# Performance work log

Hardware: AMD Instinct MI355X
Metric: run time of the kernel (lower is better)

The kernel has to match this reference:

```python
import jax, jax.numpy as jnp
import numpy as np

B, S, D_MODEL, H = 4, 2048, 1024, 16
DEPTH = D_MODEL // H          # 64
HD = DEPTH // 2               # 32, per-head projection dim
SCALE = float(np.sqrt(DEPTH))  # note: sqrt(full depth), as in the torch code
NEG = -1e10


def setup_inputs() -> dict:
    key = jax.random.key(0)
    kq, kk, kv, km, kwq, kwk, kwv, kwo = jax.random.split(key, 8)
    q = jax.random.normal(kq, (B, S, D_MODEL), dtype=jnp.float32)
    k = jax.random.normal(kk, (B, S, D_MODEL), dtype=jnp.float32)
    v = jax.random.normal(kv, (B, S, D_MODEL), dtype=jnp.float32)
    attention_mask = jax.random.uniform(km, (B, S, S)) < 0.1
    # xavier-uniform-ish init; stacked per-head weights [H, d_model, hd]
    lim_qkv = float(np.sqrt(6.0 / (D_MODEL + HD)))
    Wq = jax.random.uniform(kwq, (H, D_MODEL, HD), minval=-lim_qkv, maxval=lim_qkv)
    Wk = jax.random.uniform(kwk, (H, D_MODEL, HD), minval=-lim_qkv, maxval=lim_qkv)
    Wv = jax.random.uniform(kwv, (H, D_MODEL, HD), minval=-lim_qkv, maxval=lim_qkv)
    lim_o = float(np.sqrt(6.0 / (H * HD + D_MODEL)))
    Wo = jax.random.uniform(kwo, (H * HD, D_MODEL), minval=-lim_o, maxval=lim_o)
    return {"q": q, "k": k, "v": v, "attention_mask": attention_mask,
            "Wq": Wq, "Wk": Wk, "Wv": Wv, "Wo": Wo}


def reference(q, k, v, attention_mask, Wq, Wk, Wv, Wo):
    # batched per-head projections (equivalent to the per-head Linear loop)
    Q = jnp.einsum('bsd,hde->bhse', q, Wq)   # [B,H,S,hd]
    K = jnp.einsum('bsd,hde->bhse', k, Wk)
    V = jnp.einsum('bsd,hde->bhse', v, Wv)
    scores = jnp.einsum('bhqe,bhke->bhqk', Q, K) / SCALE  # [B,H,S,S]
    scores = jnp.where(attention_mask[:, None, :, :], NEG, scores)
    attn = jax.nn.softmax(scores, axis=-1)
    z = jnp.einsum('bhqk,bhke->bhqe', attn, V)            # [B,H,S,hd]
    # concat heads along last dim (head order matches torch cat)
    multi = z.transpose(0, 2, 1, 3).reshape(q.shape[0], q.shape[1], H * HD)
    out = multi @ Wo                                       # [B,S,d_model]
    return out  # dropout p=0.0 (eval) is identity
```

## Files before the change

### kernel.cpp

```cpp
#include <hip/hip_runtime.h>
#include <hip/hip_bf16.h>
#include <math.h>

typedef unsigned short u16;
typedef unsigned int u32;
typedef unsigned long long u64;
typedef __attribute__((ext_vector_type(8))) short s16x8;
typedef __attribute__((ext_vector_type(4))) short s16x4;
typedef __attribute__((ext_vector_type(4))) float f32x4;
typedef __attribute__((ext_vector_type(16))) float f32x16;
typedef __attribute__((ext_vector_type(2))) unsigned int u32x2;

#define DEV static __device__ __forceinline__

DEV u16 f2bf(float f){
  __hip_bfloat16 h = __float2bfloat16(f);
  return *reinterpret_cast<u16*>(&h);
}

DEV u32 cvt_pk_bf16(float lo, float hi_){
  u32 r;
  asm("v_cvt_pk_bf16_f32 %0, %1, %2" : "=v"(r) : "v"(lo), "v"(hi_));
  return r;
}

DEV u32x2 pl32swap(u32 a, u32 b){
  return __builtin_amdgcn_permlane32_swap(a, b, false, false);
}

template<int CPOS> DEV float mzero(float p, u32 msn){
  int ext;
  asm("v_bfe_i32 %0, %1, %2, 1" : "=v"(ext) : "v"(msn), "n"(CPOS));
  return __uint_as_float(__float_as_uint(p) & (u32)ext);
}

__global__ void detect_mask_kernel(const unsigned char* __restrict__ m, int* __restrict__ flag){
  __shared__ int cnt;
  if (threadIdx.x==0) cnt=0;
  __syncthreads();
  int nz=0;
  for (int i=threadIdx.x;i<4096;i+=256) nz += (m[(size_t)i*4+1]!=0)?1:0;
  if (nz) atomicAdd(&cnt, nz);
  __syncthreads();
  if (threadIdx.x==0) *flag = (cnt==0)?4:1;
}

__global__ __launch_bounds__(256) void pack_mask_kernel(const unsigned char* __restrict__ m,
    const int* __restrict__ flag, u16* __restrict__ mb16){
  const int stride = *flag;
  const size_t gid = (size_t)blockIdx.x*256u + threadIdx.x;
  u32 bits = 0;
  if (stride == 1){
    const uint4 v = *(const uint4*)(m + gid*16);
    bits  =  ((v.x & 0x01010101u) * 0x01020408u) >> 24;
    bits |= (((v.y & 0x01010101u) * 0x01020408u) >> 24) << 4;
    bits |= (((v.z & 0x01010101u) * 0x01020408u) >> 24) << 8;
    bits |= (((v.w & 0x01010101u) * 0x01020408u) >> 24) << 12;
  } else {
    const unsigned char* mm = m + gid*64;
    const uint4 a = *(const uint4*)(mm);
    const uint4 b = *(const uint4*)(mm+16);
    const uint4 c = *(const uint4*)(mm+32);
    const uint4 d = *(const uint4*)(mm+48);
    bits  = (u32)(a.x!=0) | ((u32)(a.y!=0)<<1) | ((u32)(a.z!=0)<<2) | ((u32)(a.w!=0)<<3)
          | ((u32)(b.x!=0)<<4) | ((u32)(b.y!=0)<<5) | ((u32)(b.z!=0)<<6) | ((u32)(b.w!=0)<<7)
          | ((u32)(c.x!=0)<<8) | ((u32)(c.y!=0)<<9) | ((u32)(c.z!=0)<<10)| ((u32)(c.w!=0)<<11)
          | ((u32)(d.x!=0)<<12)| ((u32)(d.y!=0)<<13)| ((u32)(d.z!=0)<<14)| ((u32)(d.w!=0)<<15);
  }
  mb16[gid] = (u16)bits;
}

__global__ __launch_bounds__(256) void prep_weights_kernel(
    const float* __restrict__ Wq, const float* __restrict__ Wk, const float* __restrict__ Wv,
    const float* __restrict__ Wo, u16* __restrict__ WT, u16* __restrict__ WoT){
  int gid = blockIdx.x*256 + threadIdx.x;
  if (gid < 3*512*1024){
    int z = gid >> 19;
    int r = gid & ((1<<19)-1);
    int n = r >> 10, d = r & 1023;
    const float* W = (z==0)?Wq:((z==1)?Wk:Wv);
    int h = n>>5, e = n&31;
    float wv = W[((size_t)h*1024 + (size_t)d)*32 + e];
    if (z==0) wv *= 0.18033688011112042f;
    WT[gid] = f2bf(wv);
  } else {
    int r = gid - 3*512*1024;
    int n = r >> 9, cc = r & 511;
    WoT[r] = f2bf(Wo[(size_t)cc*1024 + n]);
  }
}

__global__ __launch_bounds__(256) void gemm_proj_kernel(
    const float* __restrict__ Aq, const float* __restrict__ Ak, const float* __restrict__ Av,
    const u16* __restrict__ WT, u16* __restrict__ Qp, u16* __restrict__ Kp, u16* __restrict__ Vt)
{
  __shared__ u16 As[128*64];
  __shared__ u16 Bs[128*64];
  const int z = blockIdx.z;
  const float* __restrict__ A = (z==0)?Aq:((z==1)?Ak:Av);
  const u16* __restrict__ W = WT + (size_t)z*(512*1024);
  const int m0 = blockIdx.x*128, n0 = blockIdx.y*128;
  const int t = threadIdx.x, lane = t&63, wv = t>>6;
  const int wr = wv>>1, wc = wv&1;
  const int c = lane&15, g = lane>>4;
  f32x4 acc[4][4] = {};
  for (int kk=0; kk<1024; kk+=64){
    #pragma unroll
    for (int j=0;j<8;j++){
      int idx = t + j*256;
      int row = idx>>4, kq=(idx&15)<<2;
      f32x4 a4 = *(const f32x4*)(A + (size_t)(m0+row)*1024 + kk + kq);
      s16x4 b4;
      b4[0]=(short)f2bf(a4[0]); b4[1]=(short)f2bf(a4[1]);
      b4[2]=(short)f2bf(a4[2]); b4[3]=(short)f2bf(a4[3]);
      int co = (kq<<1) ^ ((row&7)<<4);
      *(s16x4*)((char*)As + row*128 + co) = b4;
    }
    #pragma unroll
    for (int j=0;j<4;j++){
      int idx = t + j*256;
      int n = idx>>3, k8=(idx&7)<<3;
      s16x8 bv = *(const s16x8*)(W + (size_t)(n0+n)*1024 + kk + k8);
      int co = (k8<<1) ^ ((n&7)<<4);
      *(s16x8*)((char*)Bs + n*128 + co) = bv;
    }
    __syncthreads();
    #pragma unroll
    for (int ks=0;ks<2;ks++){
      s16x8 af[4], bf[4];
      #pragma unroll
      for (int i=0;i<4;i++){
        int ra = wr*64 + i*16 + c;
        af[i] = *(const s16x8*)((const char*)As + ra*128 + ((ks*64 + g*16) ^ ((ra&7)<<4)));
        int rb = wc*64 + i*16 + c;
        bf[i] = *(const s16x8*)((const char*)Bs + rb*128 + ((ks*64 + g*16) ^ ((rb&7)<<4)));
      }
      #pragma unroll
      for (int mi=0;mi<4;mi++)
        #pragma unroll
        for (int nj=0;nj<4;nj++)
          acc[mi][nj] = __builtin_amdgcn_mfma_f32_16x16x32_bf16(af[mi], bf[nj], acc[mi][nj], 0, 0, 0);
    }
    __syncthreads();
  }
  #pragma unroll
  for (int mi=0;mi<4;mi++){
    #pragma unroll
    for (int nj=0;nj<4;nj++){
      #pragma unroll
      for (int r=0;r<4;r++){
        int gm = m0 + wr*64 + mi*16 + g*4 + r;
        int gn = n0 + wc*64 + nj*16 + c;
        u16 val = f2bf(acc[mi][nj][r]);
        int b = gm>>11, s = gm&2047, hh = gn>>5, e = gn&31;
        if (z==0)      Qp[((size_t)(b*16+hh)*2048 + s)*32 + e] = val;
        else if (z==1) Kp[((size_t)(b*16+hh)*2048 + s)*32 + e] = val;
        else           Vt[((size_t)(b*16+hh)*32 + e)*2048 + s] = val;
      }
    }
  }
}

__global__ __launch_bounds__(256, 4) void attn_kernel(
    const u16* __restrict__ Qp, const u16* __restrict__ Kp, const u16* __restrict__ Vt,
    const u32* __restrict__ mb32, u16* __restrict__ Z)
{
  __shared__ float Osh[4][32][36];
  const int t = threadIdx.x, lane = t&63, wid = t>>6;
  const int c = lane&31, hi = lane>>5;
  const int hi8 = hi*8;
  const int wg = blockIdx.x;
  const int xcd = wg & 7, loc = wg >> 3;
  const int bh = xcd*8 + (loc>>4);
  const int qb = loc & 15;
  const int b = bh>>4, h = bh&15;
  const int q0 = qb*128 + wid*32;
  const u16* Qh = Qp + (size_t)bh*2048*32;
  const u16* Kh = Kp + (size_t)bh*2048*32;
  const u16* Vh = Vt + (size_t)bh*32*2048;

  const s16x8 qf0 = *(const s16x8*)(Qh + (size_t)(q0 + c)*32 + hi8);
  const s16x8 qf1 = *(const s16x8*)(Qh + (size_t)(q0 + c)*32 + 16 + hi8);

  union { u32 u[4]; s16x8 v; } ones_u = {{0x3F803F80u,0x3F803F80u,0x3F803F80u,0x3F803F80u}};
  const s16x8 ones = ones_u.v;

  const f32x16 z16 = {0,0,0,0,0,0,0,0,0,0,0,0,0,0,0,0};
  f32x16 O = z16, L = z16;
  const u32* mrowp = mb32 + ((size_t)b*2048 + (size_t)(q0 + c))*64;

  #pragma unroll 2
  for (int kt = 0; kt < 64; ++kt){
    const int kb = kt*32;
    const u16* kbase = Kh + (size_t)(kb + c)*32 + hi8;
    const s16x8 kf0 = *(const s16x8*)(kbase);
    const s16x8 kf1 = *(const s16x8*)(kbase + 16);
    const u16* vbase = Vh + (size_t)c*2048 + kb + hi8;
    const s16x8 vf0 = *(const s16x8*)(vbase);
    const s16x8 vf1 = *(const s16x8*)(vbase + 16);
    const u32 msn = ~(mrowp[kt] >> (4*hi));

    f32x16 p = __builtin_amdgcn_mfma_f32_32x32x16_bf16(kf0, qf0, z16, 0, 0, 0);
    p = __builtin_amdgcn_mfma_f32_32x32x16_bf16(kf1, qf1, p, 0, 0, 0);

    #define MZE(R) p[R] = mzero<(((R)&3)+8*((R)>>2))>(__builtin_amdgcn_exp2f(p[R]), msn)
    MZE(0);  MZE(1);  MZE(2);  MZE(3);
    MZE(4);  MZE(5);  MZE(6);  MZE(7);
    MZE(8);  MZE(9);  MZE(10); MZE(11);
    MZE(12); MZE(13); MZE(14); MZE(15);
    #undef MZE

    u32 pw0 = cvt_pk_bf16(p[0],  p[1]);
    u32 pw1 = cvt_pk_bf16(p[2],  p[3]);
    u32 pw2 = cvt_pk_bf16(p[4],  p[5]);
    u32 pw3 = cvt_pk_bf16(p[6],  p[7]);
    u32 pw4 = cvt_pk_bf16(p[8],  p[9]);
    u32 pw5 = cvt_pk_bf16(p[10], p[11]);
    u32 pw6 = cvt_pk_bf16(p[12], p[13]);
    u32 pw7 = cvt_pk_bf16(p[14], p[15]);
    u32x2 a02 = pl32swap(pw0, pw2);
    u32x2 a13 = pl32swap(pw1, pw3);
    u32x2 a46 = pl32swap(pw4, pw6);
    u32x2 a57 = pl32swap(pw5, pw7);
    union { u32 u[4]; s16x8 v; } fA0 = {{a02[0], a13[0], a02[1], a13[1]}};
    union { u32 u[4]; s16x8 v; } fA1 = {{a46[0], a57[0], a46[1], a57[1]}};

    O = __builtin_amdgcn_mfma_f32_32x32x16_bf16(vf0, fA0.v, O, 0, 0, 0);
    O = __builtin_amdgcn_mfma_f32_32x32x16_bf16(vf1, fA1.v, O, 0, 0, 0);
    L = __builtin_amdgcn_mfma_f32_32x32x16_bf16(ones, fA0.v, L, 0, 0, 0);
    L = __builtin_amdgcn_mfma_f32_32x32x16_bf16(ones, fA1.v, L, 0, 0, 0);
  }

  const float linv = 1.0f / L[0];
  #pragma unroll
  for (int r=0;r<16;r++){
    const int hd = (r&3) + 8*(r>>2) + 4*hi;
    Osh[wid][c][hd] = O[r] * linv;
  }
  __syncthreads();
  const int rq = lane >> 1, rc0 = (lane & 1)*16;
  const float* orow = &Osh[wid][rq][0];
  union { u16 q[8]; s16x8 v; } o0, o1;
  #pragma unroll
  for (int j=0;j<8;j++){ o0.q[j] = f2bf(orow[rc0+j]); o1.q[j] = f2bf(orow[rc0+8+j]); }
  u16* zp = Z + ((size_t)b*2048 + (size_t)(q0 + rq))*512 + h*32 + rc0;
  *(s16x8*)(zp)   = o0.v;
  *(s16x8*)(zp+8) = o1.v;
}

__global__ __launch_bounds__(256) void gemm_out_kernel(
    const u16* __restrict__ Zb, const u16* __restrict__ WoT, float* __restrict__ out)
{
  __shared__ u16 As[128*64];
  __shared__ u16 Bs[128*64];
  const int m0 = blockIdx.x*128, n0 = blockIdx.y*128;
  const int t = threadIdx.x, lane=t&63, wv=t>>6;
  const int wr=wv>>1, wc=wv&1, c=lane&15, g=lane>>4;
  f32x4 acc[4][4] = {};
  for (int kk=0; kk<512; kk+=64){
    #pragma unroll
    for (int j=0;j<4;j++){
      int idx = t + j*256;
      int row = idx>>3, k8=(idx&7)<<3;
      int co = (k8<<1) ^ ((row&7)<<4);
      s16x8 av = *(const s16x8*)(Zb + (size_t)(m0+row)*512 + kk + k8);
      *(s16x8*)((char*)As + row*128 + co) = av;
      s16x8 bv = *(const s16x8*)(WoT + (size_t)(n0+row)*512 + kk + k8);
      *(s16x8*)((char*)Bs + row*128 + co) = bv;
    }
    __syncthreads();
    #pragma unroll
    for (int ks=0;ks<2;ks++){
      s16x8 af[4], bf[4];
      #pragma unroll
      for (int i=0;i<4;i++){
        int ra = wr*64 + i*16 + c;
        af[i] = *(const s16x8*)((const char*)As + ra*128 + ((ks*64 + g*16) ^ ((ra&7)<<4)));
        int rb = wc*64 + i*16 + c;
        bf[i] = *(const s16x8*)((const char*)Bs + rb*128 + ((ks*64 + g*16) ^ ((rb&7)<<4)));
      }
      #pragma unroll
      for (int mi=0;mi<4;mi++)
        #pragma unroll
        for (int nj=0;nj<4;nj++)
          acc[mi][nj] = __builtin_amdgcn_mfma_f32_16x16x32_bf16(af[mi], bf[nj], acc[mi][nj], 0, 0, 0);
    }
    __syncthreads();
  }
  #pragma unroll
  for (int mi=0;mi<4;mi++)
    #pragma unroll
    for (int nj=0;nj<4;nj++)
      #pragma unroll
      for (int r=0;r<4;r++){
        int gm = m0 + wr*64 + mi*16 + g*4 + r;
        int gn = n0 + wc*64 + nj*16 + c;
        out[(size_t)gm*1024 + gn] = acc[mi][nj][r];
      }
}

extern "C" void kernel_launch(void* const* d_in, const int* in_sizes, int n_in,
                              void* d_out, int out_size, void* d_ws, size_t ws_size,
                              hipStream_t stream)
{
  const float* q  = (const float*)d_in[0];
  const float* k  = (const float*)d_in[1];
  const float* v  = (const float*)d_in[2];
  const unsigned char* mask = (const unsigned char*)d_in[3];
  const float* Wq = (const float*)d_in[4];
  const float* Wk = (const float*)d_in[5];
  const float* Wv = (const float*)d_in[6];
  const float* Wo = (const float*)d_in[7];
  float* out = (float*)d_out;

  char* ws = (char*)d_ws;
  u16* Qp  = (u16*)(ws);
  u16* Kp  = (u16*)(ws + 8388608);
  u16* Vt  = (u16*)(ws + 16777216);
  u16* Z   = (u16*)(ws + 25165824);
  u16* WT  = (u16*)(ws + 33554432);
  u16* WoT = (u16*)(ws + 36700160);
  u16* mb16 = (u16*)(ws + 37748736);
  int* flag = (int*)(ws + 39845888);

  detect_mask_kernel<<<1, 256, 0, stream>>>(mask, flag);
  pack_mask_kernel<<<4096, 256, 0, stream>>>(mask, flag, mb16);
  prep_weights_kernel<<<8192, 256, 0, stream>>>(Wq, Wk, Wv, Wo, WT, WoT);
  gemm_proj_kernel<<<dim3(64,4,3), 256, 0, stream>>>(q, k, v, WT, Qp, Kp, Vt);
  attn_kernel<<<1024, 256, 0, stream>>>(Qp, Kp, Vt, (const u32*)mb16, Z);
  gemm_out_kernel<<<dim3(64,8), 256, 0, stream>>>(Z, WoT, out);
  (void)in_sizes; (void)n_in; (void)out_size; (void)ws_size;
}
```

Before: 220.8 us.

## Split attention key range across two waves per query tile and combine in LDS

Each 32-row query tile is now handled by two waves, each covering half of the key tiles. Their partial O and L accumulators are summed through shared memory before normalisation. The grid doubles to 2048 blocks and the launch bound asks for 8 blocks per CU, which shortens each wave's serial loop and exposes more parallelism. The cost is extra LDS traffic, an additional barrier, and half the waves sitting idle during the epilogue. This relies on the kernel not subtracting a running max, so the two halves can be added without rescaling.

```diff
diff --git a/kernel.cpp b/kernel.cpp
--- a/kernel.cpp
+++ b/kernel.cpp
@@ -161,20 +161,23 @@
   }
 }
 
-__global__ __launch_bounds__(256, 4) void attn_kernel(
+__global__ __launch_bounds__(256, 8) void attn_kernel(
     const u16* __restrict__ Qp, const u16* __restrict__ Kp, const u16* __restrict__ Vt,
     const u32* __restrict__ mb32, u16* __restrict__ Z)
 {
-  __shared__ float Osh[4][32][36];
+  __shared__ float Psh[2][32][33];
+  __shared__ float Tsh[2][32][33];
+  __shared__ float Lsh[2][32];
   const int t = threadIdx.x, lane = t&63, wid = t>>6;
   const int c = lane&31, hi = lane>>5;
   const int hi8 = hi*8;
+  const int qt = wid>>1, kh = wid&1;
   const int wg = blockIdx.x;
   const int xcd = wg & 7, loc = wg >> 3;
-  const int bh = xcd*8 + (loc>>4);
-  const int qb = loc & 15;
+  const int bh = xcd*8 + (loc>>5);
+  const int qg = loc & 31;
   const int b = bh>>4, h = bh&15;
-  const int q0 = qb*128 + wid*32;
+  const int q0 = qg*64 + qt*32;
   const u16* Qh = Qp + (size_t)bh*2048*32;
   const u16* Kh = Kp + (size_t)bh*2048*32;
   const u16* Vh = Vt + (size_t)bh*32*2048;
@@ -188,9 +191,10 @@
   const f32x16 z16 = {0,0,0,0,0,0,0,0,0,0,0,0,0,0,0,0};
   f32x16 O = z16, L = z16;
   const u32* mrowp = mb32 + ((size_t)b*2048 + (size_t)(q0 + c))*64;
+  const int kt0 = kh*32;
 
   #pragma unroll 2
-  for (int kt = 0; kt < 64; ++kt){
+  for (int kt = kt0; kt < kt0 + 32; ++kt){
     const int kb = kt*32;
     const u16* kbase = Kh + (size_t)(kb + c)*32 + hi8;
     const s16x8 kf0 = *(const s16x8*)(kbase);
@@ -231,21 +235,34 @@
     L = __builtin_amdgcn_mfma_f32_32x32x16_bf16(ones, fA1.v, L, 0, 0, 0);
   }
 
-  const float linv = 1.0f / L[0];
-  #pragma unroll
-  for (int r=0;r<16;r++){
-    const int hd = (r&3) + 8*(r>>2) + 4*hi;
-    Osh[wid][c][hd] = O[r] * linv;
+  if (kh == 1){
+    #pragma unroll
+    for (int r=0;r<16;r++){
+      const int hd = (r&3) + 8*(r>>2) + 4*hi;
+      Psh[qt][c][hd] = O[r];
+    }
+    if (hi == 0) Lsh[qt][c] = L[0];
   }
   __syncthreads();
-  const int rq = lane >> 1, rc0 = (lane & 1)*16;
-  const float* orow = &Osh[wid][rq][0];
-  union { u16 q[8]; s16x8 v; } o0, o1;
-  #pragma unroll
-  for (int j=0;j<8;j++){ o0.q[j] = f2bf(orow[rc0+j]); o1.q[j] = f2bf(orow[rc0+8+j]); }
-  u16* zp = Z + ((size_t)b*2048 + (size_t)(q0 + rq))*512 + h*32 + rc0;
-  *(s16x8*)(zp)   = o0.v;
-  *(s16x8*)(zp+8) = o1.v;
+  if (kh == 0){
+    const float linv = 1.0f / (L[0] + Lsh[qt][c]);
+    #pragma unroll
+    for (int r=0;r<16;r++){
+      const int hd = (r&3) + 8*(r>>2) + 4*hi;
+      Tsh[qt][c][hd] = (O[r] + Psh[qt][c][hd]) * linv;
+    }
+  }
+  __syncthreads();
+  if (kh == 0){
+    const int rq = lane >> 1, rc0 = (lane & 1)*16;
+    const float* orow = &Tsh[qt][rq][0];
+    union { u16 q[8]; s16x8 v; } o0, o1;
+    #pragma unroll
+    for (int j=0;j<8;j++){ o0.q[j] = f2bf(orow[rc0+j]); o1.q[j] = f2bf(orow[rc0+8+j]); }
+    u16* zp = Z + ((size_t)b*2048 + (size_t)(q0 + rq))*512 + h*32 + rc0;
+    *(s16x8*)(zp)   = o0.v;
+    *(s16x8*)(zp+8) = o1.v;
+  }
 }
 
 __global__ __launch_bounds__(256) void gemm_out_kernel(
@@ -327,7 +344,7 @@
   pack_mask_kernel<<<4096, 256, 0, stream>>>(mask, flag, mb16);
   prep_weights_kernel<<<8192, 256, 0, stream>>>(Wq, Wk, Wv, Wo, WT, WoT);
   gemm_proj_kernel<<<dim3(64,4,3), 256, 0, stream>>>(q, k, v, WT, Qp, Kp, Vt);
-  attn_kernel<<<1024, 256, 0, stream>>>(Qp, Kp, Vt, (const u32*)mb16, Z);
+  attn_kernel<<<2048, 256, 0, stream>>>(Qp, Kp, Vt, (const u32*)mb16, Z);
   gemm_out_kernel<<<dim3(64,8), 256, 0, stream>>>(Z, WoT, out);
   (void)in_sizes; (void)n_in; (void)out_size; (void)ws_size;
 }
```

Measured after the change: 539.3 us. +144.2%, slower.
